# Performance work log

Hardware: AMD Instinct MI355X
Metric: run time of the kernel (lower is better)

## Reference

```python
import jax, jax.numpy as jnp
import numpy as np

N = 100000; C = 128; H = 8; G = C // 4
B = 2; Z = 40; Y = 996; X = 996
WIN = 12; NUM_WIN = 200; EPS = 1e-3


def _make_indices():
    rng = np.random.RandomState(0)
    total = B * Z * Y * X
    uk = np.unique(rng.randint(0, total, size=300000).astype(np.int64))[:N]
    b = uk // (Z * Y * X); r = uk % (Z * Y * X)
    z = r // (Y * X); r = r % (Y * X)
    y = r // X; x = r % X
    return b, z, y, x, uk


def _neighbors(b, z, y, x, keys, offsets):
    # submanifold conv: output only at active sites; lookup coord+offset in active set
    sk = np.sort(keys); order = np.argsort(keys)
    cols = []
    for dz, dy, dx in offsets:
        nz, ny, nx = z + dz, y + dy, x + dx
        valid = (nz >= 0) & (nz < Z) & (ny >= 0) & (ny < Y) & (nx >= 0) & (nx < X)
        cand = ((b * Z + nz) * Y + ny) * X + nx
        pos = np.searchsorted(sk, cand)
        posc = np.minimum(pos, N - 1)
        found = valid & (sk[posc] == cand)
        cols.append(np.where(found, order[posc], N))  # N = sentinel (zero row)
    return np.stack(cols, axis=1).astype(np.int32)


def setup_inputs() -> dict:
    b, z, y, x, keys = _make_indices()
    off_k = [(dz, dy, dx) for dz in (-1, 0, 1) for dy in (-1, 0, 1) for dx in (-1, 0, 1)]
    off_h = [(0, 0, d) for d in range(-6, 7)]  # kernel (1,1,13) along x
    off_w = [(0, d, 0) for d in range(-6, 7)]  # kernel (1,13,1) along y
    nbr_k = _neighbors(b, z, y, x, keys, off_k)
    nbr_h = _neighbors(b, z, y, x, keys, off_h)
    nbr_w = _neighbors(b, z, y, x, keys, off_w)
    coords = np.stack([y, x], axis=0)
    wis = []
    for d in range(2):
        wkey = b * 1000 + coords[d] // WIN
        _, inv = np.unique(wkey, return_inverse=True)
        wis.append(inv)
    win_inds = np.stack(wis, 0).astype(np.int32)

    ks = jax.random.split(jax.random.key(0), 20)
    s = 0.05
    return dict(
        feats=jax.random.normal(ks[0], (N, C), jnp.float32),
        win_inds=jnp.asarray(win_inds),
        nbr_k=jnp.asarray(nbr_k), nbr_h=jnp.asarray(nbr_h), nbr_w=jnp.asarray(nbr_w),
        bn_g=jnp.ones((2, C)) + s * jax.random.normal(ks[1], (2, C)),
        bn_b=s * jax.random.normal(ks[2], (2, C)),
        Wqkv=s * jax.random.normal(ks[3], (2, C, 3 * C)),
        Wproj=s * jax.random.normal(ks[4], (2, C, C)),
        bproj=s * jax.random.normal(ks[5], (2, C)),
        bn1_g=jnp.ones((2, C)) + s * jax.random.normal(ks[6], (2, C)),
        bn1_b=s * jax.random.normal(ks[7], (2, C)),
        Wk=s * jax.random.normal(ks[8], (2, 27, G, G)),
        Wh=s * jax.random.normal(ks[9], (2, 13, G, G)),
        Ww=s * jax.random.normal(ks[10], (2, 13, G, G)),
        bn2_g=jnp.ones((2, C)) + s * jax.random.normal(ks[11], (2, C)),
        bn2_b=s * jax.random.normal(ks[12], (2, C)),
        fc1_W=s * jax.random.normal(ks[13], (2, C, 2 * C)),
        fc1_b=s * jax.random.normal(ks[14], (2, 2 * C)),
        fc2_W=s * jax.random.normal(ks[15], (2, 2 * C, C)),
        fc2_b=s * jax.random.normal(ks[16], (2, C)),
    )


def _bn(x, g, b):
    # BatchNorm1d, training-mode batch statistics, eps=1e-3
    m = jnp.mean(x, 0)
    v = jnp.var(x, 0)
    return (x - m) * jax.lax.rsqrt(v + EPS) * g + b


def _attn(x, wi, Wqkv, Wp, bp):
    # windowed linear attention: per-window K^T V + normalization by sum(K)
    q, k, v = jnp.split(x @ Wqkv, 3, axis=1)
    q = jax.nn.relu(q).reshape(N, H, C // H)
    k = jax.nn.relu(k).reshape(N, H, C // H)
    v = v.reshape(N, H, C // H)
    kv = jax.ops.segment_sum(jnp.einsum('nhc,nhd->nhcd', k, v), wi, NUM_WIN)
    s = jax.ops.segment_sum(k, wi, NUM_WIN)
    y = jnp.einsum('nhc,nhcd->nhd', q, kv[wi])
    z = jnp.sum(s[wi] * q, -1, keepdims=True)
    y = (y / (z + EPS)).reshape(N, C)
    return y @ Wp + bp


def _subm(f, nbr, W):
    # submanifold sparse conv via precomputed neighbor map (sentinel row = zeros)
    fp = jnp.concatenate([f, jnp.zeros((1, f.shape[1]), f.dtype)], 0)
    return jnp.einsum('nkc,kcd->nd', fp[nbr], W)


def reference(feats, win_inds, nbr_k, nbr_h, nbr_w, bn_g, bn_b, Wqkv, Wproj, bproj,
              bn1_g, bn1_b, Wk, Wh, Ww, bn2_g, bn2_b, fc1_W, fc1_b, fc2_W, fc2_b):
    f = feats
    for d in range(2):  # directions
        x = _attn(_bn(f, bn_g[d], bn_b[d]), win_inds[d], Wqkv[d], Wproj[d], bproj[d])
        f = f + x
        # CWI_FFN_Layer_3D
        fb = _bn(f, bn1_g[d], bn1_b[d])
        f2 = jnp.concatenate([
            _subm(fb[:, :G], nbr_k, Wk[d]),
            _subm(fb[:, G:2 * G], nbr_h, Wh[d]),
            _subm(fb[:, 2 * G:3 * G], nbr_w, Ww[d]),
            fb[:, 3 * G:],
        ], axis=1)
        f = fb + f2
        h = _bn(f, bn2_g[d], bn2_b[d])
        f = f + (jax.nn.relu(h @ fc1_W[d] + fc1_b[d]) @ fc2_W[d] + fc2_b[d])
    return f
```

## Files before the change

### kernel.cpp

```cpp
#include <hip/hip_runtime.h>
#include <math.h>

#define NPTS 100000
#define CCH 128
#define NWIN 200
#define NBLK_STATS 512
#define NBLK_GEMM 782
#define NBLK_SORT 391
#define SEGSZ 128
#define NSEG_MAX 1024

#define BM 128
#define BN 128
#define BK 64

typedef __attribute__((ext_vector_type(8))) short bf16x8;
typedef __attribute__((ext_vector_type(4))) float f32x4;
typedef __attribute__((ext_vector_type(4))) unsigned short u16x4;

__device__ __forceinline__ unsigned short f2bf(float f) {
    union { float f; unsigned u; } x; x.f = f;
    unsigned r = x.u + 0x7fff + ((x.u >> 16) & 1);
    return (unsigned short)(r >> 16);
}
__device__ __forceinline__ float bf2f(unsigned short h) {
    union { unsigned u; float f; } x; x.u = ((unsigned)h) << 16;
    return x.f;
}

__global__ __launch_bounds__(256) void copy_stats(const float* __restrict__ src,
                                                  float* __restrict__ F,
                                                  float* __restrict__ part) {
    int t = threadIdx.x;
    int b = blockIdx.x;
    int rg = t >> 5;
    int c4 = (t & 31) * 4;
    float s0=0.f,s1=0.f,s2=0.f,s3=0.f,q0=0.f,q1=0.f,q2=0.f,q3=0.f;
    for (int n = b * 8 + rg; n < NPTS; n += NBLK_STATS * 8) {
        float4 v = *reinterpret_cast<const float4*>(&src[(size_t)n * CCH + c4]);
        *reinterpret_cast<float4*>(&F[(size_t)n * CCH + c4]) = v;
        s0 += v.x; s1 += v.y; s2 += v.z; s3 += v.w;
        q0 += v.x*v.x; q1 += v.y*v.y; q2 += v.z*v.z; q3 += v.w*v.w;
    }
    __shared__ float red[8][256];
    red[rg][c4+0] = s0; red[rg][c4+1] = s1; red[rg][c4+2] = s2; red[rg][c4+3] = s3;
    red[rg][128+c4+0] = q0; red[rg][128+c4+1] = q1; red[rg][128+c4+2] = q2; red[rg][128+c4+3] = q3;
    __syncthreads();
    float a = 0.f;
#pragma unroll
    for (int g = 0; g < 8; g++) a += red[g][t];
    part[b * 256 + t] = a;
}

__global__ __launch_bounds__(256) void bn_partial(const float* __restrict__ F,
                                                  float* __restrict__ part) {
    int t = threadIdx.x;
    int b = blockIdx.x;
    int rg = t >> 5;
    int c4 = (t & 31) * 4;
    float s0=0.f,s1=0.f,s2=0.f,s3=0.f,q0=0.f,q1=0.f,q2=0.f,q3=0.f;
    for (int n = b * 8 + rg; n < NPTS; n += NBLK_STATS * 8) {
        float4 v = *reinterpret_cast<const float4*>(&F[(size_t)n * CCH + c4]);
        s0 += v.x; s1 += v.y; s2 += v.z; s3 += v.w;
        q0 += v.x*v.x; q1 += v.y*v.y; q2 += v.z*v.z; q3 += v.w*v.w;
    }
    __shared__ float red[8][256];
    red[rg][c4+0] = s0; red[rg][c4+1] = s1; red[rg][c4+2] = s2; red[rg][c4+3] = s3;
    red[rg][128+c4+0] = q0; red[rg][128+c4+1] = q1; red[rg][128+c4+2] = q2; red[rg][128+c4+3] = q3;
    __syncthreads();
    float a = 0.f;
#pragma unroll
    for (int g = 0; g < 8; g++) a += red[g][t];
    part[b * 256 + t] = a;
}

__global__ __launch_bounds__(256) void bnred_k(const float* __restrict__ part,
                                               float* __restrict__ part2, int nblk) {
    int t = threadIdx.x;
    int i = blockIdx.x;
    int chunk = (nblk + 15) >> 4;
    float a = 0.f;
    for (int j = 0; j < chunk; j++) {
        int idx = i * chunk + j;
        if (idx < nblk) a += part[(size_t)idx * 256 + t];
    }
    part2[i * 256 + t] = a;
}

__global__ void bn_finalize(const float* __restrict__ part2,
                            const float* __restrict__ g, const float* __restrict__ bb,
                            float* __restrict__ scale, float* __restrict__ shift) {
    int c = threadIdx.x;
    double s = 0.0, q = 0.0;
#pragma unroll
    for (int b = 0; b < 16; b++) {
        s += (double)part2[b * 256 + c];
        q += (double)part2[b * 256 + 128 + c];
    }
    double m = s / (double)NPTS;
    double var = q / (double)NPTS - m * m;
    double rstd = 1.0 / sqrt(var + 1e-3);
    float sc = (float)rstd * g[c];
    scale[c] = sc;
    shift[c] = bb[c] - (float)m * sc;
}

__global__ __launch_bounds__(128) void wprep(
    const float* __restrict__ W, int K, int N,
    const float* __restrict__ sc, const float* __restrict__ sh,
    const float* __restrict__ bias,
    unsigned short* __restrict__ WT, float* __restrict__ biasf)
{
    int n = blockIdx.x;
    int t = threadIdx.x;
    float part = 0.f;
    for (int k = t; k < K; k += 128) {
        float w = W[(size_t)k * N + n];
        float s = sc ? sc[k] * w : w;
        WT[(size_t)n * K + k] = f2bf(s);
        if (sh) part += sh[k] * w;
    }
    __shared__ float red[128];
    red[t] = part;
    __syncthreads();
    for (int o = 64; o > 0; o >>= 1) {
        if (t < o) red[t] += red[t + o];
        __syncthreads();
    }
    if (t == 0) biasf[n] = red[0] + (bias ? bias[n] : 0.f);
}

__global__ void wconv_prep_all(const float* __restrict__ Wk, const float* __restrict__ Wh,
                               const float* __restrict__ Ww, unsigned short* __restrict__ WB) {
    int i = blockIdx.x * 256 + threadIdx.x;
    if (i >= 53 * 1024) return;
    int tap = i >> 10; int rem = i & 1023; int dd = rem >> 5; int c = rem & 31;
    const float* src; int lt;
    if (tap < 27)      { src = Wk; lt = tap; }
    else if (tap < 40) { src = Wh; lt = tap - 27; }
    else               { src = Ww; lt = tap - 40; }
    WB[i] = f2bf(src[lt * 1024 + c * 32 + dd]);
}

template<int NT>
__global__ __launch_bounds__(256) void gemm_knt(
    const float* __restrict__ A, int lda,
    const unsigned short* __restrict__ WT, const float* __restrict__ biasf,
    unsigned short* __restrict__ Out, int ldo, int reluLim)
{
    __shared__ __align__(16) char smem[49152];
    unsigned short* As = (unsigned short*)smem;
    unsigned short* Bs = (unsigned short*)(smem + 32768);

    const int tid  = threadIdx.x;
    const int wave = tid >> 6;
    const int lane = tid & 63;
    const int bm = blockIdx.x * BM;
    const int lrow = lane & 15;
    const int lhk  = lane >> 4;

#pragma unroll
    for (int pass = 0; pass < 16; pass++) {
        int row = pass * 8 + (tid >> 5);
        int grow = bm + row;
        int c4 = (tid & 31) * 4;
        float4 v = make_float4(0.f, 0.f, 0.f, 0.f);
        if (grow < NPTS)
            v = *reinterpret_cast<const float4*>(&A[(size_t)grow * lda + c4]);
        u16x4 h4 = { f2bf(v.x), f2bf(v.y), f2bf(v.z), f2bf(v.w) };
        int half = c4 >> 6;
        int cw = c4 & 63;
        int sw = (cw >> 3) ^ (row & 7);
        *reinterpret_cast<u16x4*>(&As[row * 128 + half * 64 + sw * 8 + (cw & 7)]) = h4;
    }

    for (int nt = 0; nt < NT; nt++) {
        const int bn = nt * BN;
        f32x4 acc[2][8];
#pragma unroll
        for (int i = 0; i < 2; i++)
#pragma unroll
            for (int j = 0; j < 8; j++)
                acc[i][j] = (f32x4){0.f, 0.f, 0.f, 0.f};

#pragma unroll
        for (int h = 0; h < 2; h++) {
            __syncthreads();
#pragma unroll
            for (int pass = 0; pass < 4; pass++) {
                int n = pass * 32 + (tid >> 3);
                bf16x8 w = *reinterpret_cast<const bf16x8*>(
                    &WT[(size_t)(bn + n) * 128 + h * 64 + (tid & 7) * 8]);
                int sw = (tid & 7) ^ (n & 7);
                *reinterpret_cast<bf16x8*>(&Bs[n * 64 + sw * 8]) = w;
            }
            __syncthreads();
#pragma unroll
            for (int ks = 0; ks < 2; ks++) {
                bf16x8 af[2], bfr[8];
#pragma unroll
                for (int fi = 0; fi < 2; fi++) {
                    int row = wave * 32 + fi * 16 + lrow;
                    int sw = (ks * 4 + lhk) ^ (row & 7);
                    af[fi] = *reinterpret_cast<const bf16x8*>(&As[row * 128 + h * 64 + sw * 8]);
                }
#pragma unroll
                for (int fj = 0; fj < 8; fj++) {
                    int col = fj * 16 + lrow;
                    int sw = (ks * 4 + lhk) ^ (col & 7);
                    bfr[fj] = *reinterpret_cast<const bf16x8*>(&Bs[col * 64 + sw * 8]);
                }
#pragma unroll
                for (int fi = 0; fi < 2; fi++)
#pragma unroll
                    for (int fj = 0; fj < 8; fj++)
                        acc[fi][fj] = __builtin_amdgcn_mfma_f32_16x16x32_bf16(
                            af[fi], bfr[fj], acc[fi][fj], 0, 0, 0);
            }
        }

#pragma unroll
        for (int fi = 0; fi < 2; fi++) {
            int rbase = bm + wave * 32 + fi * 16 + lhk * 4;
#pragma unroll
            for (int fj = 0; fj < 8; fj++) {
                int col = bn + fj * 16 + lrow;
                float bv = biasf[col];
                bool rl = col < reluLim;
#pragma unroll
                for (int r = 0; r < 4; r++) {
                    int rr = rbase + r;
                    if (rr < NPTS) {
                        float v = acc[fi][fj][r] + bv;
                        if (rl) v = fmaxf(v, 0.f);
                        Out[(size_t)rr * ldo + col] = f2bf(v);
                    }
                }
            }
        }
    }
}

__global__ __launch_bounds__(256) void gemm_res(
    const unsigned short* __restrict__ Ab, int lda,
    const unsigned short* __restrict__ WT, const float* __restrict__ biasf,
    int K,
    float* __restrict__ Outp, int ldo,
    float* __restrict__ partOut)
{
    __shared__ __align__(16) char smem[34048];
    unsigned short* As = (unsigned short*)smem;
    unsigned short* Bs = As + BM * BK;
    float* Ep = (float*)smem;

    const int tid  = threadIdx.x;
    const int wave = tid >> 6;
    const int lane = tid & 63;
    const int bm = blockIdx.y * BM;
    const int bn = 0;

    f32x4 acc[2][8];
#pragma unroll
    for (int i = 0; i < 2; i++)
#pragma unroll
        for (int j = 0; j < 8; j++)
            acc[i][j] = (f32x4){0.f, 0.f, 0.f, 0.f};

    const int lrow = lane & 15;
    const int lhk  = lane >> 4;

    for (int kk = 0; kk < K; kk += BK) {
#pragma unroll
        for (int pass = 0; pass < 4; pass++) {
            int row = pass * 32 + (tid >> 3);
            int grow = bm + row;
            bf16x8 w = (bf16x8){0,0,0,0,0,0,0,0};
            if (grow < NPTS)
                w = *reinterpret_cast<const bf16x8*>(&Ab[(size_t)grow * lda + kk + (tid & 7) * 8]);
            int sw = (tid & 7) ^ (row & 7);
            *reinterpret_cast<bf16x8*>(&As[row * 64 + sw * 8]) = w;
        }
#pragma unroll
        for (int pass = 0; pass < 4; pass++) {
            int n = pass * 32 + (tid >> 3);
            bf16x8 w = *reinterpret_cast<const bf16x8*>(&WT[(size_t)(bn + n) * K + kk + (tid & 7) * 8]);
            int sw = (tid & 7) ^ (n & 7);
            *reinterpret_cast<bf16x8*>(&Bs[n * 64 + sw * 8]) = w;
        }
        __syncthreads();

#pragma unroll
        for (int ks = 0; ks < 2; ks++) {
            bf16x8 af[2], bfr[8];
#pragma unroll
            for (int fi = 0; fi < 2; fi++) {
                int row = wave * 32 + fi * 16 + lrow;
                int sw = (ks * 4 + lhk) ^ (row & 7);
                af[fi] = *reinterpret_cast<const bf16x8*>(&As[row * 64 + sw * 8]);
            }
#pragma unroll
            for (int fj = 0; fj < 8; fj++) {
                int col = fj * 16 + lrow;
                int sw = (ks * 4 + lhk) ^ (col & 7);
                bfr[fj] = *reinterpret_cast<const bf16x8*>(&Bs[col * 64 + sw * 8]);
            }
#pragma unroll
            for (int fi = 0; fi < 2; fi++)
#pragma unroll
                for (int fj = 0; fj < 8; fj++)
                    acc[fi][fj] = __builtin_amdgcn_mfma_f32_16x16x32_bf16(
                        af[fi], bfr[fj], acc[fi][fj], 0, 0, 0);
        }
        __syncthreads();
    }

    float s0=0.f,s1=0.f,s2=0.f,s3=0.f,q0=0.f,q1=0.f,q2=0.f,q3=0.f;
    for (int hh = 0; hh < 2; hh++) {
        if ((wave >> 1) == hh) {
#pragma unroll
            for (int fi = 0; fi < 2; fi++) {
                int row = (wave & 1) * 32 + fi * 16 + (lane >> 4) * 4;
#pragma unroll
                for (int fj = 0; fj < 8; fj++) {
                    int col = fj * 16 + (lane & 15);
#pragma unroll
                    for (int r = 0; r < 4; r++)
                        Ep[(row + r) * 132 + col] = acc[fi][fj][r];
                }
            }
        }
        __syncthreads();
#pragma unroll
        for (int pass = 0; pass < 8; pass++) {
            int idx = pass * 256 + tid;
            int r = idx >> 5;
            int c4 = (idx & 31) * 4;
            int rr = bm + hh * 64 + r;
            if (rr < NPTS) {
                float4 v = *reinterpret_cast<const float4*>(&Ep[r * 132 + c4]);
                float4 b = *reinterpret_cast<const float4*>(&biasf[c4]);
                v.x += b.x; v.y += b.y; v.z += b.z; v.w += b.w;
                float* o = &Outp[(size_t)rr * ldo + c4];
                float4 ov = *reinterpret_cast<const float4*>(o);
                v.x += ov.x; v.y += ov.y; v.z += ov.z; v.w += ov.w;
                *reinterpret_cast<float4*>(o) = v;
                s0 += v.x; s1 += v.y; s2 += v.z; s3 += v.w;
                q0 += v.x*v.x; q1 += v.y*v.y; q2 += v.z*v.z; q3 += v.w*v.w;
            }
        }
        __syncthreads();
    }
    if (partOut) {
        float* red = (float*)smem;
        int rg = tid >> 5;
        int c4 = (tid & 31) * 4;
        red[rg * 256 + c4 + 0] = s0; red[rg * 256 + c4 + 1] = s1;
        red[rg * 256 + c4 + 2] = s2; red[rg * 256 + c4 + 3] = s3;
        red[rg * 256 + 128 + c4 + 0] = q0; red[rg * 256 + 128 + c4 + 1] = q1;
        red[rg * 256 + 128 + c4 + 2] = q2; red[rg * 256 + 128 + c4 + 3] = q3;
        __syncthreads();
        float a = 0.f;
#pragma unroll
        for (int g = 0; g < 8; g++) a += red[g * 256 + tid];
        partOut[(size_t)blockIdx.y * 256 + tid] = a;
    }
}

__global__ __launch_bounds__(256) void hist2_k(const int* __restrict__ wi,
                                               int* __restrict__ BH) {
    __shared__ int h[NWIN];
    int t = threadIdx.x;
    if (t < NWIN) h[t] = 0;
    __syncthreads();
    int n = blockIdx.x * 256 + t;
    if (n < NPTS) atomicAdd(&h[wi[n]], 1);
    __syncthreads();
    if (t < NWIN) BH[blockIdx.x * 256 + t] = h[t];
}

__global__ __launch_bounds__(256) void colscan2_k(const int* __restrict__ BH,
                                                  int* __restrict__ OFFB,
                                                  int* __restrict__ TOT) {
    int w = blockIdx.x;
    int t = threadIdx.x;
    __shared__ int s[512];
    int v0 = (t < NBLK_SORT) ? BH[t * 256 + w] : 0;
    int v1 = (t + 256 < NBLK_SORT) ? BH[(t + 256) * 256 + w] : 0;
    s[t] = v0; s[t + 256] = v1;
    __syncthreads();
#pragma unroll
    for (int off = 1; off < 512; off <<= 1) {
        int a0 = (t >= off) ? s[t - off] : 0;
        int a1 = (t + 256 >= off) ? s[t + 256 - off] : 0;
        __syncthreads();
        s[t] += a0;
        s[t + 256] += a1;
        __syncthreads();
    }
    if (t < NBLK_SORT) OFFB[t * 256 + w] = s[t] - v0;
    if (t + 256 < NBLK_SORT) OFFB[(t + 256) * 256 + w] = s[t + 256] - v1;
    if (t == 0) TOT[w] = s[NBLK_SORT - 1];
}

__global__ __launch_bounds__(256) void meta2_k(const int* __restrict__ TOT,
                                               int* __restrict__ OFFS,
                                               int* __restrict__ SEGW, int* __restrict__ SEGP0,
                                               int* __restrict__ SEGP1, int* __restrict__ SEGBASE) {
    __shared__ int offs[NWIN + 1];
    __shared__ int segc[NWIN];
    int t = threadIdx.x;
    if (t < NWIN) segc[t] = TOT[t];
    __syncthreads();
    if (t == 0) {
        int a = 0;
        for (int w = 0; w < NWIN; w++) { int c = segc[w]; offs[w] = a; a += c; }
        offs[NWIN] = a;
    }
    __syncthreads();
    if (t <= NWIN) OFFS[t] = offs[t];
    if (t < NWIN) segc[t] = (offs[t + 1] - offs[t] + SEGSZ - 1) / SEGSZ;
    __syncthreads();
    if (t == 0) {
        int a = 0;
        for (int i = 0; i < NWIN; i++) { int c = segc[i]; segc[i] = a; SEGBASE[i] = a; a += c; }
        SEGBASE[NWIN] = a;
    }
    __syncthreads();
    if (t < NWIN) {
        int b = segc[t];
        int p0 = offs[t], p1 = offs[t + 1];
        for (int p = p0; p < p1; p += SEGSZ) {
            SEGW[b] = t; SEGP0[b] = p; SEGP1[b] = min(p + SEGSZ, p1); b++;
        }
    }
}

__global__ __launch_bounds__(256) void scatter2_k(const int* __restrict__ wi,
                                                  const int* __restrict__ OFFS,
                                                  const int* __restrict__ OFFB,
                                                  int* __restrict__ list) {
    __shared__ int h[NWIN];
    int t = threadIdx.x;
    if (t < NWIN) h[t] = 0;
    __syncthreads();
    int n = blockIdx.x * 256 + t;
    if (n < NPTS) {
        int w = wi[n];
        int r = atomicAdd(&h[w], 1);
        list[OFFS[w] + OFFB[blockIdx.x * 256 + w] + r] = n;
    }
}

__global__ __launch_bounds__(256) void window_kv_seg(
    const unsigned short* __restrict__ R0bf,
    const int* __restrict__ list,
    const int* __restrict__ SEGP0, const int* __restrict__ SEGP1,
    const int* __restrict__ SEGBASE,
    float* __restrict__ PKV)
{
    int sid = blockIdx.x;
    if (sid >= SEGBASE[NWIN]) return;
    int t = threadIdx.x;
    int p0 = SEGP0[sid], p1 = SEGP1[sid];
    __shared__ float buf[8][256];
    float acc[8] = {0.f,0.f,0.f,0.f,0.f,0.f,0.f,0.f};
    float sa = 0.f;
    int f0 = t * 8;
    int h = f0 >> 8;
    int c = (f0 >> 4) & 15;
    int d0 = f0 & 15;
    const int sr = t >> 5;
    const int c8 = (t & 31) * 8;

    for (int g = p0; g < p1; g += 8) {
        int m = min(8, p1 - g);
        int nj[8];
#pragma unroll
        for (int j = 0; j < 8; j++)
            nj[j] = list[(g + j < p1) ? g + j : p1 - 1];
        __syncthreads();
        {
            const unsigned short* row = &R0bf[(size_t)nj[sr] * 384 + 128];
            bf16x8 hv = *reinterpret_cast<const bf16x8*>(&row[c8]);
            float4 lo = make_float4(bf2f((unsigned short)hv[0]), bf2f((unsigned short)hv[1]),
                                    bf2f((unsigned short)hv[2]), bf2f((unsigned short)hv[3]));
            float4 hi = make_float4(bf2f((unsigned short)hv[4]), bf2f((unsigned short)hv[5]),
                                    bf2f((unsigned short)hv[6]), bf2f((unsigned short)hv[7]));
            *reinterpret_cast<float4*>(&buf[sr][c8]) = lo;
            *reinterpret_cast<float4*>(&buf[sr][c8 + 4]) = hi;
        }
        __syncthreads();
#pragma unroll
        for (int j = 0; j < 8; j++) {
            if (j >= m) break;
            float kc = buf[j][h * 16 + c];
#pragma unroll
            for (int i = 0; i < 8; i++) acc[i] += kc * buf[j][128 + h * 16 + d0 + i];
            if (t < 128) sa += buf[j][t];
        }
    }
    float* out = &PKV[(size_t)sid * 2176];
#pragma unroll
    for (int i = 0; i < 8; i++) out[f0 + i] = acc[i];
    if (t < 128) out[2048 + t] = sa;
}

__global__ __launch_bounds__(256) void kv_reduce(
    const float* __restrict__ PKV, const int* __restrict__ SEGBASE,
    float* __restrict__ KV, float* __restrict__ SB)
{
    int w = blockIdx.x;
    int t = threadIdx.x;
    int s0 = SEGBASE[w], s1 = SEGBASE[w + 1];
    float a[8] = {0.f,0.f,0.f,0.f,0.f,0.f,0.f,0.f};
    float sb = 0.f;
    for (int s = s0; s < s1; s++) {
        const float* p = &PKV[(size_t)s * 2176];
#pragma unroll
        for (int i = 0; i < 8; i++) a[i] += p[t * 8 + i];
        if (t < 128) sb += p[2048 + t];
    }
#pragma unroll
    for (int i = 0; i < 8; i++) KV[w * 2048 + t * 8 + i] = a[i];
    if (t < 128) SB[w * 128 + t] = sb;
}

__global__ __launch_bounds__(256) void attn_y_seg(
    const unsigned short* __restrict__ R0bf,
    unsigned short* __restrict__ Ybf,
    const int* __restrict__ list,
    const int* __restrict__ SEGW, const int* __restrict__ SEGP0,
    const int* __restrict__ SEGP1, const int* __restrict__ SEGBASE,
    const float* __restrict__ KV, const float* __restrict__ SB)
{
    int sid = blockIdx.x;
    if (sid >= SEGBASE[NWIN]) return;
    int t = threadIdx.x;
    int w = SEGW[sid];
    int g  = t >> 5;
    int h  = (t >> 2) & 7;
    int d4 = (t & 3) * 4;

    float4 kvr[16];
    const float* kvb = &KV[w * 2048 + h * 256 + d4];
#pragma unroll
    for (int cc = 0; cc < 16; cc++)
        kvr[cc] = *reinterpret_cast<const float4*>(&kvb[cc * 16]);
    float sreg[16];
    const float* sb = &SB[w * 128 + h * 16];
#pragma unroll
    for (int cc = 0; cc < 16; cc++) sreg[cc] = sb[cc];

    int p0 = SEGP0[sid], p1 = SEGP1[sid];
    for (int p = p0 + g; p < p1; p += 8) {
        int n = list[p];
        const unsigned short* q = &R0bf[(size_t)n * 384 + h * 16];
        bf16x8 qa = *reinterpret_cast<const bf16x8*>(&q[0]);
        bf16x8 qb = *reinterpret_cast<const bf16x8*>(&q[8]);
        float qq[16];
#pragma unroll
        for (int i = 0; i < 8; i++) {
            qq[i] = bf2f((unsigned short)qa[i]);
            qq[8 + i] = bf2f((unsigned short)qb[i]);
        }
        float z = 0.f;
        float4 y = make_float4(0.f, 0.f, 0.f, 0.f);
#pragma unroll
        for (int cc = 0; cc < 16; cc++) {
            z += qq[cc] * sreg[cc];
            y.x += qq[cc] * kvr[cc].x;
            y.y += qq[cc] * kvr[cc].y;
            y.z += qq[cc] * kvr[cc].z;
            y.w += qq[cc] * kvr[cc].w;
        }
        float inv = 1.f / (z + 1e-3f);
        u16x4 o = { f2bf(y.x * inv), f2bf(y.y * inv), f2bf(y.z * inv), f2bf(y.w * inv) };
        *reinterpret_cast<u16x4*>(&Ybf[(size_t)n * 128 + h * 16 + d4]) = o;
    }
}

__global__ void bn_apply(float* F, unsigned short* __restrict__ FBbf,
                         const float* __restrict__ scale, const float* __restrict__ shift)
{
    int i = blockIdx.x * 256 + threadIdx.x;
    int n = i >> 5;
    int c4 = (i & 31) * 4;
    float4 v = *reinterpret_cast<const float4*>(&F[n * CCH + c4]);
    float4 o;
    o.x = v.x * scale[c4 + 0] + shift[c4 + 0];
    o.y = v.y * scale[c4 + 1] + shift[c4 + 1];
    o.z = v.z * scale[c4 + 2] + shift[c4 + 2];
    o.w = v.w * scale[c4 + 3] + shift[c4 + 3];
    u16x4 hv = { f2bf(o.x), f2bf(o.y), f2bf(o.z), f2bf(o.w) };
    *reinterpret_cast<u16x4*>(&FBbf[(size_t)n * 128 + c4]) = hv;
    if (c4 >= 96) {
        float4 t = make_float4(2.f * o.x, 2.f * o.y, 2.f * o.z, 2.f * o.w);
        *reinterpret_cast<float4*>(&F[n * CCH + c4]) = t;
    }
}

template<int KN>
__global__ __launch_bounds__(256) void conv_direct(
    const int* __restrict__ nbrA, const int* __restrict__ nbrB,
    const unsigned short* __restrict__ WBall, int wbBase,
    const unsigned short* __restrict__ FBbf,
    float* __restrict__ F, int offBase)
{
    const int which = blockIdx.y;
    const int* __restrict__ nbr = which ? nbrB : nbrA;
    const int off = offBase + which * 32;
    const unsigned short* __restrict__ WB = WBall + wbBase + which * KN * 1024;

    __shared__ __align__(16) float Ep[128 * 36];

    const int tid = threadIdx.x;
    const int wave = tid >> 6;
    const int lane = tid & 63;
    const int bm = blockIdx.x * 128;
    const int lrow = lane & 15;
    const int lk = lane >> 4;

    const int row0 = bm + wave * 32 + lrow;
    const int row1 = row0 + 16;

    f32x4 acc[2][2];
#pragma unroll
    for (int i = 0; i < 2; i++)
#pragma unroll
        for (int j = 0; j < 2; j++)
            acc[i][j] = (f32x4){0.f, 0.f, 0.f, 0.f};

    constexpr int CHK = (KN == 27) ? 9 : 13;
    for (int c0 = 0; c0 < KN; c0 += CHK) {
        int i0[CHK], i1[CHK];
#pragma unroll
        for (int j = 0; j < CHK; j++) {
            i0[j] = (row0 < NPTS) ? nbr[(size_t)row0 * KN + c0 + j] : NPTS;
            i1[j] = (row1 < NPTS) ? nbr[(size_t)row1 * KN + c0 + j] : NPTS;
        }
#pragma unroll
        for (int j = 0; j < CHK; j++) {
            int k = c0 + j;
            bf16x8 a0 = (bf16x8){0,0,0,0,0,0,0,0};
            bf16x8 a1 = (bf16x8){0,0,0,0,0,0,0,0};
            if (i0[j] < NPTS)
                a0 = *reinterpret_cast<const bf16x8*>(&FBbf[(size_t)i0[j] * 128 + off + lk * 8]);
            if (i1[j] < NPTS)
                a1 = *reinterpret_cast<const bf16x8*>(&FBbf[(size_t)i1[j] * 128 + off + lk * 8]);
            bf16x8 b0 = *reinterpret_cast<const bf16x8*>(&WB[k * 1024 + lrow * 32 + lk * 8]);
            bf16x8 b1 = *reinterpret_cast<const bf16x8*>(&WB[k * 1024 + (16 + lrow) * 32 + lk * 8]);
            acc[0][0] = __builtin_amdgcn_mfma_f32_16x16x32_bf16(a0, b0, acc[0][0], 0, 0, 0);
            acc[0][1] = __builtin_amdgcn_mfma_f32_16x16x32_bf16(a0, b1, acc[0][1], 0, 0, 0);
            acc[1][0] = __builtin_amdgcn_mfma_f32_16x16x32_bf16(a1, b0, acc[1][0], 0, 0, 0);
            acc[1][1] = __builtin_amdgcn_mfma_f32_16x16x32_bf16(a1, b1, acc[1][1], 0, 0, 0);
        }
    }

#pragma unroll
    for (int fi = 0; fi < 2; fi++)
#pragma unroll
        for (int fj = 0; fj < 2; fj++) {
            int r0 = wave * 32 + fi * 16 + lk * 4;
            int col = fj * 16 + lrow;
#pragma unroll
            for (int r = 0; r < 4; r++)
                Ep[(r0 + r) * 36 + col] = acc[fi][fj][r];
        }
    __syncthreads();
#pragma unroll
    for (int pass = 0; pass < 4; pass++) {
        int idx = pass * 256 + tid;
        int r = idx >> 3;
        int c4 = (idx & 7) * 4;
        int rr = bm + r;
        if (rr < NPTS) {
            float4 v = *reinterpret_cast<const float4*>(&Ep[r * 36 + c4]);
            u16x4 fbh = *reinterpret_cast<const u16x4*>(&FBbf[(size_t)rr * 128 + off + c4]);
            v.x += bf2f(fbh.x); v.y += bf2f(fbh.y);
            v.z += bf2f(fbh.z); v.w += bf2f(fbh.w);
            *reinterpret_cast<float4*>(&F[(size_t)rr * CCH + off + c4]) = v;
        }
    }
}

extern "C" void kernel_launch(void* const* d_in, const int* in_sizes, int n_in,
                              void* d_out, int out_size, void* d_ws, size_t ws_size,
                              hipStream_t stream)
{
    const float* feats   = (const float*)d_in[0];
    const int*   win_inds= (const int*)d_in[1];
    const int*   nbr_k   = (const int*)d_in[2];
    const int*   nbr_h   = (const int*)d_in[3];
    const int*   nbr_w   = (const int*)d_in[4];
    const float* bn_g    = (const float*)d_in[5];
    const float* bn_b    = (const float*)d_in[6];
    const float* Wqkv    = (const float*)d_in[7];
    const float* Wproj   = (const float*)d_in[8];
    const float* bproj   = (const float*)d_in[9];
    const float* bn1_g   = (const float*)d_in[10];
    const float* bn1_b   = (const float*)d_in[11];
    const float* Wk      = (const float*)d_in[12];
    const float* Wh      = (const float*)d_in[13];
    const float* Ww      = (const float*)d_in[14];
    const float* bn2_g   = (const float*)d_in[15];
    const float* bn2_b   = (const float*)d_in[16];
    const float* fc1_W   = (const float*)d_in[17];
    const float* fc1_b   = (const float*)d_in[18];
    const float* fc2_W   = (const float*)d_in[19];
    const float* fc2_b   = (const float*)d_in[20];

    float* F  = (float*)d_out;
    float* KV = (float*)d_ws;
    float* SB = KV + NWIN * 2048;
    float* ST = SB + NWIN * 128;
    float* PART = ST + 768;
    float* PART2 = PART + (size_t)NBLK_GEMM * 256;
    float* PKV = PART2 + 16 * 256;
    int* OFFS = (int*)(PKV + (size_t)NSEG_MAX * 2176);
    int* TOT  = OFFS + 256;
    int* LIST = TOT + 256;
    int* BH   = LIST + 100096;
    int* OFFB = BH + NBLK_SORT * 256;
    int* SEGW = OFFB + NBLK_SORT * 256;
    int* SEGP0= SEGW + NSEG_MAX;
    int* SEGP1= SEGP0 + NSEG_MAX;
    int* SEGBASE = SEGP1 + NSEG_MAX;
    unsigned short* WQKVT = (unsigned short*)(SEGBASE + 256);
    unsigned short* WPROJT = WQKVT + 384 * 128;
    unsigned short* WFC1T  = WPROJT + 128 * 128;
    unsigned short* WFC2T  = WFC1T + 256 * 128;
    float* BQKV  = (float*)(WFC2T + 128 * 256);
    float* BPROJ = BQKV + 384;
    float* BFC1  = BPROJ + 128;
    float* BFC2  = BFC1 + 256;
    unsigned short* R0bf = (unsigned short*)(BFC2 + 128);
    unsigned short* Hbf  = R0bf;
    unsigned short* Ybf  = R0bf + (size_t)NPTS * 384;
    unsigned short* FBbf = Ybf + (size_t)NPTS * 128;
    unsigned short* WBall= FBbf + (size_t)NPTS * 128;

    copy_stats<<<NBLK_STATS, 256, 0, stream>>>(feats, F, PART);

    dim3 g1(1, NBLK_GEMM);
    dim3 gc13(NBLK_GEMM, 2);

    for (int d = 0; d < 2; d++) {
        const int* wi = win_inds + (size_t)d * NPTS;
        float* SC0 = ST, *SH0 = ST + 128, *SC1 = ST + 256, *SH1 = ST + 384,
             * SC2 = ST + 512, *SH2 = ST + 640;

        bnred_k<<<16, 256, 0, stream>>>(PART, PART2, d == 0 ? NBLK_STATS : NBLK_GEMM);
        bn_finalize<<<1, 128, 0, stream>>>(PART2, bn_g + d * CCH, bn_b + d * CCH, SC0, SH0);
        wprep<<<384, 128, 0, stream>>>(Wqkv + (size_t)d * CCH * 384, 128, 384,
                                       SC0, SH0, nullptr, WQKVT, BQKV);
        wprep<<<128, 128, 0, stream>>>(Wproj + (size_t)d * CCH * CCH, 128, 128,
                                       nullptr, nullptr, bproj + d * CCH, WPROJT, BPROJ);
        wconv_prep_all<<<212, 256, 0, stream>>>(Wk + (size_t)d * 27 * 1024,
                                                Wh + (size_t)d * 13 * 1024,
                                                Ww + (size_t)d * 13 * 1024, WBall);

        gemm_knt<3><<<NBLK_GEMM, 256, 0, stream>>>(F, CCH, WQKVT, BQKV, R0bf, 384, 256);

        hist2_k<<<NBLK_SORT, 256, 0, stream>>>(wi, BH);
        colscan2_k<<<NWIN, 256, 0, stream>>>(BH, OFFB, TOT);
        meta2_k<<<1, 256, 0, stream>>>(TOT, OFFS, SEGW, SEGP0, SEGP1, SEGBASE);
        scatter2_k<<<NBLK_SORT, 256, 0, stream>>>(wi, OFFS, OFFB, LIST);

        window_kv_seg<<<NSEG_MAX, 256, 0, stream>>>(R0bf, LIST, SEGP0, SEGP1, SEGBASE, PKV);
        kv_reduce<<<NWIN, 256, 0, stream>>>(PKV, SEGBASE, KV, SB);

        attn_y_seg<<<NSEG_MAX, 256, 0, stream>>>(R0bf, Ybf, LIST, SEGW, SEGP0, SEGP1,
                                                 SEGBASE, KV, SB);

        gemm_res<<<g1, 256, 0, stream>>>(Ybf, 128, WPROJT, BPROJ, 128, F, CCH, PART);

        bnred_k<<<16, 256, 0, stream>>>(PART, PART2, NBLK_GEMM);
        bn_finalize<<<1, 128, 0, stream>>>(PART2, bn1_g + d * CCH, bn1_b + d * CCH, SC1, SH1);
        bn_apply<<<12500, 256, 0, stream>>>(F, FBbf, SC1, SH1);

        conv_direct<27><<<NBLK_GEMM, 256, 0, stream>>>(nbr_k, nbr_k, WBall, 0, FBbf, F, 0);
        conv_direct<13><<<gc13, 256, 0, stream>>>(nbr_h, nbr_w, WBall, 27 * 1024, FBbf, F, 32);

        bn_partial<<<NBLK_STATS, 256, 0, stream>>>(F, PART);
        bnred_k<<<16, 256, 0, stream>>>(PART, PART2, NBLK_STATS);
        bn_finalize<<<1, 128, 0, stream>>>(PART2, bn2_g + d * CCH, bn2_b + d * CCH, SC2, SH2);
        wprep<<<256, 128, 0, stream>>>(fc1_W + (size_t)d * CCH * 256, 128, 256,
                                       SC2, SH2, fc1_b + d * 256, WFC1T, BFC1);
        wprep<<<128, 128, 0, stream>>>(fc2_W + (size_t)d * 256 * CCH, 256, 128,
                                       nullptr, nullptr, fc2_b + d * CCH, WFC2T, BFC2);

        gemm_knt<2><<<NBLK_GEMM, 256, 0, stream>>>(F, CCH, WFC1T, BFC1, Hbf, 256, 256);
        gemm_res<<<g1, 256, 0, stream>>>(Hbf, 256, WFC2T, BFC2, 256, F, CCH, PART);
    }
}
```

Measured before the change: 755.6 us.

## Read GEMM weight fragments directly from global memory and stage output through LDS

```diff
diff --git a/kernel.cpp b/kernel.cpp
--- a/kernel.cpp
+++ b/kernel.cpp
@@ -148,9 +148,9 @@
     const unsigned short* __restrict__ WT, const float* __restrict__ biasf,
     unsigned short* __restrict__ Out, int ldo, int reluLim)
 {
-    __shared__ __align__(16) char smem[49152];
+    __shared__ __align__(16) char smem[50176];
     unsigned short* As = (unsigned short*)smem;
-    unsigned short* Bs = (unsigned short*)(smem + 32768);
+    unsigned short* Ep = (unsigned short*)(smem + 32768);
 
     const int tid  = threadIdx.x;
     const int wave = tid >> 6;
@@ -173,6 +173,7 @@
         int sw = (cw >> 3) ^ (row & 7);
         *reinterpret_cast<u16x4*>(&As[row * 128 + half * 64 + sw * 8 + (cw & 7)]) = h4;
     }
+    __syncthreads();
 
     for (int nt = 0; nt < NT; nt++) {
         const int bn = nt * BN;
@@ -185,16 +186,6 @@
 
 #pragma unroll
         for (int h = 0; h < 2; h++) {
-            __syncthreads();
-#pragma unroll
-            for (int pass = 0; pass < 4; pass++) {
-                int n = pass * 32 + (tid >> 3);
-                bf16x8 w = *reinterpret_cast<const bf16x8*>(
-                    &WT[(size_t)(bn + n) * 128 + h * 64 + (tid & 7) * 8]);
-                int sw = (tid & 7) ^ (n & 7);
-                *reinterpret_cast<bf16x8*>(&Bs[n * 64 + sw * 8]) = w;
-            }
-            __syncthreads();
 #pragma unroll
             for (int ks = 0; ks < 2; ks++) {
                 bf16x8 af[2], bfr[8];
@@ -206,9 +197,8 @@
                 }
 #pragma unroll
                 for (int fj = 0; fj < 8; fj++) {
-                    int col = fj * 16 + lrow;
-                    int sw = (ks * 4 + lhk) ^ (col & 7);
-                    bfr[fj] = *reinterpret_cast<const bf16x8*>(&Bs[col * 64 + sw * 8]);
+                    bfr[fj] = *reinterpret_cast<const bf16x8*>(
+                        &WT[(size_t)(bn + fj * 16 + lrow) * 128 + h * 64 + ks * 32 + lhk * 8]);
                 }
 #pragma unroll
                 for (int fi = 0; fi < 2; fi++)
@@ -220,23 +210,37 @@
         }
 
 #pragma unroll
-        for (int fi = 0; fi < 2; fi++) {
-            int rbase = bm + wave * 32 + fi * 16 + lhk * 4;
-#pragma unroll
-            for (int fj = 0; fj < 8; fj++) {
-                int col = bn + fj * 16 + lrow;
-                float bv = biasf[col];
-                bool rl = col < reluLim;
-#pragma unroll
-                for (int r = 0; r < 4; r++) {
-                    int rr = rbase + r;
-                    if (rr < NPTS) {
-                        float v = acc[fi][fj][r] + bv;
-                        if (rl) v = fmaxf(v, 0.f);
-                        Out[(size_t)rr * ldo + col] = f2bf(v);
+        for (int ch = 0; ch < 2; ch++) {
+            if ((wave >> 1) == ch) {
+#pragma unroll
+                for (int fj = 0; fj < 8; fj++) {
+                    int col = fj * 16 + lrow;
+                    float bv = biasf[bn + col];
+                    bool rl = (bn + col) < reluLim;
+#pragma unroll
+                    for (int fi = 0; fi < 2; fi++) {
+#pragma unroll
+                        for (int r = 0; r < 4; r++) {
+                            int rloc = (wave & 1) * 32 + fi * 16 + lhk * 4 + r;
+                            float v = acc[fi][fj][r] + bv;
+                            if (rl) v = fmaxf(v, 0.f);
+                            Ep[rloc * 136 + col] = f2bf(v);
+                        }
                     }
                 }
             }
+            __syncthreads();
+#pragma unroll
+            for (int pass = 0; pass < 4; pass++) {
+                int idx = pass * 256 + tid;
+                int r = idx >> 4;
+                int c8 = (idx & 15) * 8;
+                int rr = bm + ch * 64 + r;
+                if (rr < NPTS)
+                    *reinterpret_cast<bf16x8*>(&Out[(size_t)rr * ldo + bn + c8]) =
+                        *reinterpret_cast<const bf16x8*>(&Ep[r * 136 + c8]);
+            }
+            __syncthreads();
         }
     }
 }
@@ -250,14 +254,12 @@
 {
     __shared__ __align__(16) char smem[34048];
     unsigned short* As = (unsigned short*)smem;
-    unsigned short* Bs = As + BM * BK;
     float* Ep = (float*)smem;
 
     const int tid  = threadIdx.x;
     const int wave = tid >> 6;
     const int lane = tid & 63;
     const int bm = blockIdx.y * BM;
-    const int bn = 0;
 
     f32x4 acc[2][8];
 #pragma unroll
@@ -280,13 +282,6 @@
             int sw = (tid & 7) ^ (row & 7);
             *reinterpret_cast<bf16x8*>(&As[row * 64 + sw * 8]) = w;
         }
-#pragma unroll
-        for (int pass = 0; pass < 4; pass++) {
-            int n = pass * 32 + (tid >> 3);
-            bf16x8 w = *reinterpret_cast<const bf16x8*>(&WT[(size_t)(bn + n) * K + kk + (tid & 7) * 8]);
-            int sw = (tid & 7) ^ (n & 7);
-            *reinterpret_cast<bf16x8*>(&Bs[n * 64 + sw * 8]) = w;
-        }
         __syncthreads();
 
 #pragma unroll
@@ -299,11 +294,9 @@
                 af[fi] = *reinterpret_cast<const bf16x8*>(&As[row * 64 + sw * 8]);
             }
 #pragma unroll
-            for (int fj = 0; fj < 8; fj++) {
-                int col = fj * 16 + lrow;
-                int sw = (ks * 4 + lhk) ^ (col & 7);
-                bfr[fj] = *reinterpret_cast<const bf16x8*>(&Bs[col * 64 + sw * 8]);
-            }
+            for (int fj = 0; fj < 8; fj++)
+                bfr[fj] = *reinterpret_cast<const bf16x8*>(
+                    &WT[(size_t)(fj * 16 + lrow) * K + kk + ks * 32 + lhk * 8]);
 #pragma unroll
             for (int fi = 0; fi < 2; fi++)
 #pragma unroll
```

Result: slower. 932.3 us (+23.4%).
